# Kernel tuning notes

Measured on AMD Instinct MI355X. Metric: run time of the kernel, lower is better.

Reference implementation:

```python
import jax, jax.numpy as jnp
import numpy as np

N_NODES = 100000
N_EDGES = 3200000
IN_F, HID, N_CLS = 512, 16, 7


def setup_inputs() -> dict:
    key = jax.random.key(0)
    k1, k2, k3, k4 = jax.random.split(key, 4)
    x = jax.random.normal(k1, (N_NODES, IN_F), dtype=jnp.float32)
    edge_index = jax.random.randint(k2, (2, N_EDGES), 0, N_NODES, dtype=jnp.int32)
    W1 = jax.random.normal(k3, (IN_F, HID), dtype=jnp.float32) * (1.0 / np.sqrt(IN_F))
    b1 = jnp.zeros((HID,), dtype=jnp.float32)
    W2 = jax.random.normal(k4, (HID, N_CLS), dtype=jnp.float32) * (1.0 / np.sqrt(HID))
    b2 = jnp.zeros((N_CLS,), dtype=jnp.float32)
    return {"x": x, "edge_index": edge_index, "W1": W1, "b1": b1, "W2": W2, "b2": b2}


def _gcn_norm(src, dst, n_nodes):
    # symmetric normalization with self-loops already included in (src, dst)
    deg = jax.ops.segment_sum(jnp.ones(dst.shape, jnp.float32), dst, num_segments=n_nodes)
    dinv = jnp.where(deg > 0, jax.lax.rsqrt(deg), 0.0)
    return dinv[src] * dinv[dst]  # [E]


def _gcn_conv(h, src, dst, norm, W, b, n_nodes):
    # transform-first (PyG GCNConv), then normalized scatter-add aggregation
    h = h @ W                                   # [N, out]
    msg = h[src] * norm[:, None]                # gather + scale, [E, out]
    out = jax.ops.segment_sum(msg, dst, num_segments=n_nodes)  # scatter-add
    return out + b


def reference(x, edge_index, W1, b1, W2, b2):
    n = x.shape[0]
    loops = jnp.arange(n, dtype=edge_index.dtype)
    src = jnp.concatenate([edge_index[0], loops])
    dst = jnp.concatenate([edge_index[1], loops])
    norm = _gcn_norm(src, dst, n)
    h = _gcn_conv(x, src, dst, norm, W1, b1, n)
    h = jax.nn.relu(h)
    out = _gcn_conv(h, src, dst, norm, W2, b2, n)
    return out
```

## Files before the change

kernel.cpp:

```cpp
#include <hip/hip_runtime.h>

#define CHUNK 8192
#define BMAX 512

typedef __attribute__((address_space(3))) unsigned int lds_u32;
typedef const __attribute__((address_space(1))) unsigned int glb_u32;

__device__ __forceinline__ void gload16(const float* g, float* l) {
    __builtin_amdgcn_global_load_lds((glb_u32*)g, (lds_u32*)l, 16, 0, 0);
}


__global__ __launch_bounds__(256) void k_coarse_hist(const int* __restrict__ dst, int E,
                                                     int* __restrict__ bc,
                                                     int* __restrict__ blockBase, int B) {
    __shared__ int cnt[BMAX];
    int t = threadIdx.x;
    cnt[t] = 0; cnt[t + 256] = 0;
    __syncthreads();
    int e0 = blockIdx.x * CHUNK;
#pragma unroll
    for (int it = 0; it < CHUNK / 256; ++it) {
        int e = e0 + it * 256 + t;
        if (e < E) atomicAdd(&cnt[dst[e] >> 8], 1);
    }
    __syncthreads();
    for (int b = t; b < B; b += 256) {
        int c = cnt[b];
        if (c > 0) blockBase[(size_t)blockIdx.x * B + b] = atomicAdd(&bc[b], c);
    }
}

__global__ void k_scan_bsums(int* bsums, int nb) {
    __shared__ int s[2][512];
    int t = threadIdx.x;
    int v = (t < nb) ? bsums[t] : 0;
    int p = 0;
    s[0][t] = v;
    __syncthreads();
    for (int off = 1; off < 512; off <<= 1) {
        s[p ^ 1][t] = s[p][t] + ((t >= off) ? s[p][t - off] : 0);
        p ^= 1;
        __syncthreads();
    }
    if (t < nb) bsums[t] = s[p][t] - v;
}


__global__ __launch_bounds__(256) void k_coarse_scatter(const int* __restrict__ src,
                                                        const int* __restrict__ dst, int E,
                                                        const int* __restrict__ bucketBase,
                                                        const int* __restrict__ blockBase, int B,
                                                        unsigned int* __restrict__ ebuf) {
    __shared__ int run[BMAX];
    int t = threadIdx.x;
    run[t] = 0; run[t + 256] = 0;
    __syncthreads();
    int e0 = blockIdx.x * CHUNK;
#pragma unroll
    for (int it = 0; it < CHUNK / 256; ++it) {
        int e = e0 + it * 256 + t;
        if (e < E) {
            int d = dst[e];
            int b = d >> 8;
            int rank = atomicAdd(&run[b], 1);
            int pos = bucketBase[b] + blockBase[(size_t)blockIdx.x * B + b] + rank;
            ebuf[pos] = ((unsigned int)(d & 255) << 24) | (unsigned int)src[e];
        }
    }
}


__global__ __launch_bounds__(256) void k_bucket_hist(const unsigned int* __restrict__ ebuf,
                                                     const int* __restrict__ bucketBase,
                                                     int E, int N, int B,
                                                     int* __restrict__ hist,
                                                     float* __restrict__ dinv) {
    __shared__ int cnt[256];
    int t = threadIdx.x;
    int b = blockIdx.x;
    cnt[t] = 0;
    __syncthreads();
    int e0 = bucketBase[b];
    int e1 = (b + 1 < B) ? bucketBase[b + 1] : E;
    for (int e = e0 + t; e < e1; e += 256) atomicAdd(&cnt[ebuf[e] >> 24], 1);
    __syncthreads();
    int node = b * 256 + t;
    if (node < N) {
        hist[node] = cnt[t];
        dinv[node] = rsqrtf((float)(cnt[t] + 1));
    }
}


__global__ __launch_bounds__(256) void k_fine_scatter(const unsigned int* __restrict__ ebuf,
                                                      const int* __restrict__ bucketBase,
                                                      const int* __restrict__ hist,
                                                      int E, int N, int B,
                                                      int* __restrict__ rowStart,
                                                      int* __restrict__ csr_src) {
    __shared__ int s[2][256];
    __shared__ int cnt[256];
    int t = threadIdx.x;
    int b = blockIdx.x;
    int node = b * 256 + t;
    int v = (node < N) ? hist[node] : 0;
    int p = 0;
    s[0][t] = v;
    __syncthreads();
    for (int off = 1; off < 256; off <<= 1) {
        s[p ^ 1][t] = s[p][t] + ((t >= off) ? s[p][t - off] : 0);
        p ^= 1;
        __syncthreads();
    }
    int rs = bucketBase[b] + s[p][t] - v;
    if (node < N) rowStart[node] = rs;
    cnt[t] = rs;
    __syncthreads();
    int e0 = bucketBase[b];
    int e1 = (b + 1 < B) ? bucketBase[b + 1] : E;
    for (int e = e0 + t; e < e1; e += 256) {
        unsigned int w = ebuf[e];
        int pos = atomicAdd(&cnt[w >> 24], 1);
        csr_src[pos] = (int)(w & 0xFFFFFFu);
    }
}


__global__ __launch_bounds__(256, 6) void k_gemm1(const float* __restrict__ x,
                                                  const float* __restrict__ W1,
                                                  const float* __restrict__ dinv,
                                                  int N, float* __restrict__ h1) {
    __shared__ float xs[2][2048];
    const int t = threadIdx.x;
    const int lane = t & 63;
    const int cq = __builtin_amdgcn_readfirstlane(t >> 6);
    const int R0 = blockIdx.x * 64;

    const float* gbase[2];
#pragma unroll
    for (int u = 0; u < 2; ++u) {
        int r = (cq * 2 + u) * 8 + (lane >> 3);
        int g = lane & 7;
        int row = R0 + r;
        if (row >= N) row = N - 1;
        gbase[u] = x + (size_t)row * 512 + ((g ^ (r & 7)) << 2);
    }

    float acc[4] = {0.f, 0.f, 0.f, 0.f};

#pragma unroll
    for (int u = 0; u < 2; ++u)
        gload16(gbase[u], &xs[0][((cq * 2 + u) * 64 + lane) * 4]);
    __syncthreads();

    const int row = lane;
    const int rs = row & 7;
    int p = 0;
    for (int ch = 0; ch < 16; ++ch) {
        if (ch + 1 < 16) {
#pragma unroll
            for (int u = 0; u < 2; ++u)
                gload16(gbase[u] + (ch + 1) * 32, &xs[p ^ 1][((cq * 2 + u) * 64 + lane) * 4]);
        }
        const float* xr = &xs[p][row * 32];
#pragma unroll
        for (int j = 0; j < 8; ++j) {
            int j4 = (j + cq * 2) & 7;
            float4 xv = *(const float4*)(xr + ((j4 ^ rs) << 2));
            float xe[4] = {xv.x, xv.y, xv.z, xv.w};
            int k = ch * 32 + j4 * 4;
#pragma unroll
            for (int d = 0; d < 4; ++d) {
                const float* wp = W1 + (k + d) * 16 + cq * 4;
#pragma unroll
                for (int c = 0; c < 4; ++c) acc[c] = fmaf(xe[d], wp[c], acc[c]);
            }
        }
        __syncthreads();
        p ^= 1;
    }

    int orow = R0 + row;
    if (orow < N) {
        float di = dinv[orow];
        *(float4*)(h1 + (size_t)orow * 16 + cq * 4) =
            make_float4(acc[0] * di, acc[1] * di, acc[2] * di, acc[3] * di);
    }
}


__global__ void k_gather1(const float* __restrict__ h1, const int* __restrict__ csr_src,
                          const int* __restrict__ rowStart, const int* __restrict__ hist,
                          const float* __restrict__ dinv, const float* __restrict__ b1,
                          int N, float* __restrict__ relu1) {
    int g = blockIdx.x * blockDim.x + threadIdx.x;
    int i = g >> 4, c = g & 15;
    if (i >= N) return;
    float ssum = h1[(size_t)i * 16 + c];
    int e0 = rowStart[i], e1 = e0 + hist[i];
    for (int e = e0; e < e1; ++e) {
        int s = csr_src[e];
        ssum += h1[(size_t)s * 16 + c];
    }
    float v = fmaf(dinv[i], ssum, b1[c]);
    relu1[(size_t)i * 16 + c] = fmaxf(v, 0.0f);
}


__global__ void k_h2(const float* __restrict__ relu1, const float* __restrict__ W2,
                     const float* __restrict__ dinv, int N, float* __restrict__ h2) {
    int i = blockIdx.x * blockDim.x + threadIdx.x;
    if (i >= N) return;
    float r[16];
#pragma unroll
    for (int q = 0; q < 4; ++q) {
        float4 v = *(const float4*)(relu1 + (size_t)i * 16 + q * 4);
        r[q * 4 + 0] = v.x; r[q * 4 + 1] = v.y; r[q * 4 + 2] = v.z; r[q * 4 + 3] = v.w;
    }
    float di = dinv[i];
#pragma unroll
    for (int c2 = 0; c2 < 7; ++c2) {
        float a = 0.0f;
#pragma unroll
        for (int c = 0; c < 16; ++c) a = fmaf(r[c], W2[c * 7 + c2], a);
        h2[(size_t)i * 7 + c2] = a * di;
    }
}


__global__ void k_gather2(const float* __restrict__ h2, const int* __restrict__ csr_src,
                          const int* __restrict__ rowStart, const int* __restrict__ hist,
                          const float* __restrict__ dinv, const float* __restrict__ b2,
                          int N, float* __restrict__ out) {
    int g = blockIdx.x * blockDim.x + threadIdx.x;
    int i = g >> 3, c = g & 7;
    if (i >= N || c >= 7) return;
    float ssum = h2[(size_t)i * 7 + c];
    int e0 = rowStart[i], e1 = e0 + hist[i];
    for (int e = e0; e < e1; ++e) {
        int s = csr_src[e];
        ssum += h2[(size_t)s * 7 + c];
    }
    out[(size_t)i * 7 + c] = fmaf(dinv[i], ssum, b2[c]);
}


extern "C" void kernel_launch(void* const* d_in, const int* in_sizes, int n_in,
                              void* d_out, int out_size, void* d_ws, size_t ws_size,
                              hipStream_t stream) {
    const float* x  = (const float*)d_in[0];
    const int*   ei = (const int*)d_in[1];
    const float* W1 = (const float*)d_in[2];
    const float* b1 = (const float*)d_in[3];
    const float* W2 = (const float*)d_in[4];
    const float* b2 = (const float*)d_in[5];
    float* out = (float*)d_out;

    const int N = in_sizes[0] / 512;
    const int E = in_sizes[1] / 2;
    const int* src = ei;
    const int* dst = ei + E;

    const int nb  = (N + 255) / 256;
    const int B   = nb;
    const int nbA = (E + CHUNK - 1) / CHUNK;
    const int nb64 = (N + 63) / 64;

    char* ws = (char*)d_ws;
    auto alloc = [&](size_t bytes) {
        char* p = ws;
        ws += (bytes + 511) & ~(size_t)511;
        return p;
    };
    int*   hist      = (int*)alloc((size_t)N * 4);
    float* dinv      = (float*)alloc((size_t)N * 4);
    int*   rowStart  = (int*)alloc((size_t)N * 4);
    int*   bc        = (int*)alloc((size_t)(B + 1) * 4);
    int*   blockBase = (int*)alloc((size_t)nbA * B * 4);
    int*   csr_src   = (int*)alloc((size_t)E * 4);
    size_t featBytes = (size_t)N * 16 * 4 * 2 + (size_t)N * 7 * 4;
    size_t ebufBytes = (size_t)E * 4;
    char* regB = alloc(featBytes > ebufBytes ? featBytes : ebufBytes);
    unsigned int* ebuf = (unsigned int*)regB;
    float* h1    = (float*)regB;
    float* relu1 = h1 + (size_t)N * 16;
    float* h2    = relu1 + (size_t)N * 16;

    hipMemsetAsync(bc, 0, (size_t)B * 4, stream);
    k_coarse_hist<<<nbA, 256, 0, stream>>>(dst, E, bc, blockBase, B);
    k_scan_bsums<<<1, 512, 0, stream>>>(bc, B);
    k_coarse_scatter<<<nbA, 256, 0, stream>>>(src, dst, E, bc, blockBase, B, ebuf);
    k_bucket_hist<<<B, 256, 0, stream>>>(ebuf, bc, E, N, B, hist, dinv);
    k_fine_scatter<<<B, 256, 0, stream>>>(ebuf, bc, hist, E, N, B, rowStart, csr_src);
    k_gemm1<<<nb64, 256, 0, stream>>>(x, W1, dinv, N, h1);
    k_gather1<<<(N * 16 + 255) / 256, 256, 0, stream>>>(h1, csr_src, rowStart, hist, dinv, b1, N, relu1);
    k_h2<<<nb, 256, 0, stream>>>(relu1, W2, dinv, N, h2);
    k_gather2<<<(N * 8 + 255) / 256, 256, 0, stream>>>(h2, csr_src, rowStart, hist, dinv, b2, N, out);
}
```

Before: 558.7 us.

## Build CSR with global atomics and triple-buffer the GEMM1 x loads

Replaces the two-level bucketed counting sort that builds the CSR with a simpler pipeline: a global-atomic degree histogram, a block-local plus block-sum scan, a finalize step, and a direct atomic scatter into csr_src. This removes the ebuf intermediate and several passes, but relies on heavily contended global atomics and on randomly scattered writes. Separately, GEMM1 moves from double to triple buffering of the x tiles, using explicit vmcnt waits and raw barriers so more loads are in flight. The CSR neighbour order within each row is now nondeterministic.

```diff
diff --git a/kernel.cpp b/kernel.cpp
--- a/kernel.cpp
+++ b/kernel.cpp
@@ -1,7 +1,4 @@
 #include <hip/hip_runtime.h>
-
-#define CHUNK 8192
-#define BMAX 512
 
 typedef __attribute__((address_space(3))) unsigned int lds_u32;
 typedef const __attribute__((address_space(1))) unsigned int glb_u32;
@@ -11,24 +8,30 @@
 }
 
 
-__global__ __launch_bounds__(256) void k_coarse_hist(const int* __restrict__ dst, int E,
-                                                     int* __restrict__ bc,
-                                                     int* __restrict__ blockBase, int B) {
-    __shared__ int cnt[BMAX];
-    int t = threadIdx.x;
-    cnt[t] = 0; cnt[t + 256] = 0;
+__global__ __launch_bounds__(256) void k_deg(const int* __restrict__ dst, int E,
+                                             int* __restrict__ hist) {
+    int stride = gridDim.x * 256;
+    for (int e = blockIdx.x * 256 + threadIdx.x; e < E; e += stride)
+        atomicAdd(&hist[dst[e]], 1);
+}
+
+__global__ __launch_bounds__(256) void k_scan_local(const int* __restrict__ hist, int N,
+                                                    int* __restrict__ rowStart,
+                                                    int* __restrict__ bsums) {
+    __shared__ int s[2][256];
+    int t = threadIdx.x, b = blockIdx.x;
+    int node = b * 256 + t;
+    int v = (node < N) ? hist[node] : 0;
+    int p = 0;
+    s[0][t] = v;
     __syncthreads();
-    int e0 = blockIdx.x * CHUNK;
-#pragma unroll
-    for (int it = 0; it < CHUNK / 256; ++it) {
-        int e = e0 + it * 256 + t;
-        if (e < E) atomicAdd(&cnt[dst[e] >> 8], 1);
-    }
-    __syncthreads();
-    for (int b = t; b < B; b += 256) {
-        int c = cnt[b];
-        if (c > 0) blockBase[(size_t)blockIdx.x * B + b] = atomicAdd(&bc[b], c);
-    }
+    for (int off = 1; off < 256; off <<= 1) {
+        s[p ^ 1][t] = s[p][t] + ((t >= off) ? s[p][t - off] : 0);
+        p ^= 1;
+        __syncthreads();
+    }
+    if (node < N) rowStart[node] = s[p][t] - v;
+    if (t == 255) bsums[b] = s[p][t];
 }
 
 __global__ void k_scan_bsums(int* bsums, int nb) {
@@ -46,83 +49,29 @@
     if (t < nb) bsums[t] = s[p][t] - v;
 }
 
-
-__global__ __launch_bounds__(256) void k_coarse_scatter(const int* __restrict__ src,
-                                                        const int* __restrict__ dst, int E,
-                                                        const int* __restrict__ bucketBase,
-                                                        const int* __restrict__ blockBase, int B,
-                                                        unsigned int* __restrict__ ebuf) {
-    __shared__ int run[BMAX];
-    int t = threadIdx.x;
-    run[t] = 0; run[t + 256] = 0;
-    __syncthreads();
-    int e0 = blockIdx.x * CHUNK;
-#pragma unroll
-    for (int it = 0; it < CHUNK / 256; ++it) {
-        int e = e0 + it * 256 + t;
-        if (e < E) {
-            int d = dst[e];
-            int b = d >> 8;
-            int rank = atomicAdd(&run[b], 1);
-            int pos = bucketBase[b] + blockBase[(size_t)blockIdx.x * B + b] + rank;
-            ebuf[pos] = ((unsigned int)(d & 255) << 24) | (unsigned int)src[e];
-        }
-    }
-}
-
-
-__global__ __launch_bounds__(256) void k_bucket_hist(const unsigned int* __restrict__ ebuf,
-                                                     const int* __restrict__ bucketBase,
-                                                     int E, int N, int B,
-                                                     int* __restrict__ hist,
-                                                     float* __restrict__ dinv) {
-    __shared__ int cnt[256];
-    int t = threadIdx.x;
-    int b = blockIdx.x;
-    cnt[t] = 0;
-    __syncthreads();
-    int e0 = bucketBase[b];
-    int e1 = (b + 1 < B) ? bucketBase[b + 1] : E;
-    for (int e = e0 + t; e < e1; e += 256) atomicAdd(&cnt[ebuf[e] >> 24], 1);
-    __syncthreads();
-    int node = b * 256 + t;
-    if (node < N) {
-        hist[node] = cnt[t];
-        dinv[node] = rsqrtf((float)(cnt[t] + 1));
-    }
-}
-
-
-__global__ __launch_bounds__(256) void k_fine_scatter(const unsigned int* __restrict__ ebuf,
-                                                      const int* __restrict__ bucketBase,
-                                                      const int* __restrict__ hist,
-                                                      int E, int N, int B,
-                                                      int* __restrict__ rowStart,
-                                                      int* __restrict__ csr_src) {
-    __shared__ int s[2][256];
-    __shared__ int cnt[256];
-    int t = threadIdx.x;
-    int b = blockIdx.x;
-    int node = b * 256 + t;
-    int v = (node < N) ? hist[node] : 0;
-    int p = 0;
-    s[0][t] = v;
-    __syncthreads();
-    for (int off = 1; off < 256; off <<= 1) {
-        s[p ^ 1][t] = s[p][t] + ((t >= off) ? s[p][t - off] : 0);
-        p ^= 1;
-        __syncthreads();
-    }
-    int rs = bucketBase[b] + s[p][t] - v;
-    if (node < N) rowStart[node] = rs;
-    cnt[t] = rs;
-    __syncthreads();
-    int e0 = bucketBase[b];
-    int e1 = (b + 1 < B) ? bucketBase[b + 1] : E;
-    for (int e = e0 + t; e < e1; e += 256) {
-        unsigned int w = ebuf[e];
-        int pos = atomicAdd(&cnt[w >> 24], 1);
-        csr_src[pos] = (int)(w & 0xFFFFFFu);
+__global__ __launch_bounds__(256) void k_finalize(int* __restrict__ rowStart,
+                                                  const int* __restrict__ bsums,
+                                                  const int* __restrict__ hist,
+                                                  int N, float* __restrict__ dinv,
+                                                  int* __restrict__ cnt) {
+    int i = blockIdx.x * 256 + threadIdx.x;
+    if (i < N) {
+        rowStart[i] += bsums[blockIdx.x];
+        dinv[i] = rsqrtf((float)(hist[i] + 1));
+        cnt[i] = 0;
+    }
+}
+
+__global__ __launch_bounds__(256) void k_csr_scatter(const int* __restrict__ src,
+                                                     const int* __restrict__ dst, int E,
+                                                     const int* __restrict__ rowStart,
+                                                     int* __restrict__ cnt,
+                                                     int* __restrict__ csr_src) {
+    int stride = gridDim.x * 256;
+    for (int e = blockIdx.x * 256 + threadIdx.x; e < E; e += stride) {
+        int d = dst[e];
+        int r = atomicAdd(&cnt[d], 1);
+        csr_src[rowStart[d] + r] = src[e];
     }
 }
 
@@ -131,7 +80,7 @@
                                                   const float* __restrict__ W1,
                                                   const float* __restrict__ dinv,
                                                   int N, float* __restrict__ h1) {
-    __shared__ float xs[2][2048];
+    __shared__ float xs[3][2048];
     const int t = threadIdx.x;
     const int lane = t & 63;
     const int cq = __builtin_amdgcn_readfirstlane(t >> 6);
@@ -150,36 +99,43 @@
     float acc[4] = {0.f, 0.f, 0.f, 0.f};
 
 #pragma unroll
-    for (int u = 0; u < 2; ++u)
-        gload16(gbase[u], &xs[0][((cq * 2 + u) * 64 + lane) * 4]);
-    __syncthreads();
+    for (int c = 0; c < 3; ++c)
+#pragma unroll
+        for (int u = 0; u < 2; ++u)
+            gload16(gbase[u] + c * 32, &xs[c][((cq * 2 + u) * 64 + lane) * 4]);
 
     const int row = lane;
     const int rs = row & 7;
-    int p = 0;
-    for (int ch = 0; ch < 16; ++ch) {
-        if (ch + 1 < 16) {
-#pragma unroll
-            for (int u = 0; u < 2; ++u)
-                gload16(gbase[u] + (ch + 1) * 32, &xs[p ^ 1][((cq * 2 + u) * 64 + lane) * 4]);
-        }
-        const float* xr = &xs[p][row * 32];
-#pragma unroll
-        for (int j = 0; j < 8; ++j) {
-            int j4 = (j + cq * 2) & 7;
-            float4 xv = *(const float4*)(xr + ((j4 ^ rs) << 2));
-            float xe[4] = {xv.x, xv.y, xv.z, xv.w};
-            int k = ch * 32 + j4 * 4;
-#pragma unroll
-            for (int d = 0; d < 4; ++d) {
-                const float* wp = W1 + (k + d) * 16 + cq * 4;
-#pragma unroll
-                for (int c = 0; c < 4; ++c) acc[c] = fmaf(xe[d], wp[c], acc[c]);
-            }
-        }
-        __syncthreads();
-        p ^= 1;
-    }
+
+#define GEMM1_BODY(CH, VM)                                                       \
+    do {                                                                         \
+        asm volatile("s_waitcnt vmcnt(" #VM ")" ::: "memory");                   \
+        __builtin_amdgcn_s_barrier();          \
+        __builtin_amdgcn_sched_barrier(0);      \
+        const float* xr = &xs[(CH) % 3][row * 32];                               \
+        _Pragma("unroll") for (int j = 0; j < 8; ++j) {                          \
+            int j4 = (j + cq * 2) & 7;                    \
+            float4 xv = *(const float4*)(xr + ((j4 ^ rs) << 2));                 \
+            float xe[4] = {xv.x, xv.y, xv.z, xv.w};                              \
+            int k = (CH) * 32 + j4 * 4;                                          \
+            _Pragma("unroll") for (int d = 0; d < 4; ++d) {                      \
+                const float* wp = W1 + (k + d) * 16 + cq * 4;        \
+                _Pragma("unroll") for (int c = 0; c < 4; ++c)                    \
+                    acc[c] = fmaf(xe[d], wp[c], acc[c]);                         \
+            }                                                                    \
+        }                                                                        \
+        __builtin_amdgcn_s_barrier();            \
+        if ((CH) + 3 < 16) {                                                     \
+            _Pragma("unroll") for (int u = 0; u < 2; ++u)                        \
+                gload16(gbase[u] + ((CH) + 3) * 32,                              \
+                        &xs[(CH) % 3][((cq * 2 + u) * 64 + lane) * 4]);          \
+        }                                                                        \
+    } while (0)
+
+    for (int ch = 0; ch < 14; ++ch) GEMM1_BODY(ch, 4);
+    GEMM1_BODY(14, 2);
+    GEMM1_BODY(15, 0);
+#undef GEMM1_BODY
 
     int orow = R0 + row;
     if (orow < N) {
@@ -262,9 +218,7 @@
     const int* src = ei;
     const int* dst = ei + E;
 
-    const int nb  = (N + 255) / 256;
-    const int B   = nb;
-    const int nbA = (E + CHUNK - 1) / CHUNK;
+    const int nb   = (N + 255) / 256;
     const int nb64 = (N + 63) / 64;
 
     char* ws = (char*)d_ws;
@@ -273,26 +227,22 @@
         ws += (bytes + 511) & ~(size_t)511;
         return p;
     };
-    int*   hist      = (int*)alloc((size_t)N * 4);
-    float* dinv      = (float*)alloc((size_t)N * 4);
-    int*   rowStart  = (int*)alloc((size_t)N * 4);
-    int*   bc        = (int*)alloc((size_t)(B + 1) * 4);
-    int*   blockBase = (int*)alloc((size_t)nbA * B * 4);
-    int*   csr_src   = (int*)alloc((size_t)E * 4);
-    size_t featBytes = (size_t)N * 16 * 4 * 2 + (size_t)N * 7 * 4;
-    size_t ebufBytes = (size_t)E * 4;
-    char* regB = alloc(featBytes > ebufBytes ? featBytes : ebufBytes);
-    unsigned int* ebuf = (unsigned int*)regB;
-    float* h1    = (float*)regB;
-    float* relu1 = h1 + (size_t)N * 16;
-    float* h2    = relu1 + (size_t)N * 16;
-
-    hipMemsetAsync(bc, 0, (size_t)B * 4, stream);
-    k_coarse_hist<<<nbA, 256, 0, stream>>>(dst, E, bc, blockBase, B);
-    k_scan_bsums<<<1, 512, 0, stream>>>(bc, B);
-    k_coarse_scatter<<<nbA, 256, 0, stream>>>(src, dst, E, bc, blockBase, B, ebuf);
-    k_bucket_hist<<<B, 256, 0, stream>>>(ebuf, bc, E, N, B, hist, dinv);
-    k_fine_scatter<<<B, 256, 0, stream>>>(ebuf, bc, hist, E, N, B, rowStart, csr_src);
+    int*   hist     = (int*)alloc((size_t)N * 4);
+    float* dinv     = (float*)alloc((size_t)N * 4);
+    int*   rowStart = (int*)alloc((size_t)N * 4);
+    int*   cnt      = (int*)alloc((size_t)N * 4);
+    int*   bsums    = (int*)alloc((size_t)(nb + 1) * 4);
+    int*   csr_src  = (int*)alloc((size_t)E * 4);
+    float* h1    = (float*)alloc((size_t)N * 16 * 4);
+    float* relu1 = (float*)alloc((size_t)N * 16 * 4);
+    float* h2    = (float*)alloc((size_t)N * 7 * 4);
+
+    hipMemsetAsync(hist, 0, (size_t)N * 4, stream);
+    k_deg<<<2048, 256, 0, stream>>>(dst, E, hist);
+    k_scan_local<<<nb, 256, 0, stream>>>(hist, N, rowStart, bsums);
+    k_scan_bsums<<<1, 512, 0, stream>>>(bsums, nb);
+    k_finalize<<<nb, 256, 0, stream>>>(rowStart, bsums, hist, N, dinv, cnt);
+    k_csr_scatter<<<2048, 256, 0, stream>>>(src, dst, E, rowStart, cnt, csr_src);
     k_gemm1<<<nb64, 256, 0, stream>>>(x, W1, dinv, N, h1);
     k_gather1<<<(N * 16 + 255) / 256, 256, 0, stream>>>(h1, csr_src, rowStart, hist, dinv, b1, N, relu1);
     k_h2<<<nb, 256, 0, stream>>>(relu1, W2, dinv, N, h2);
```

Result: slower. 759.2 us (+35.9%).
